# Performance work log

Measured on AMD Instinct MI355X. Metric: run time of the kernel, lower is better.

The kernel has to match this reference:

```python
import jax, jax.numpy as jnp
import numpy as np

NUM_EXPERTS = 16
TOP_K = 2
D_IN = 1024
D_HID = 4096
D_OUT = 1024
BATCH = 8192


def setup_inputs() -> dict:
    key = jax.random.key(0)
    ks = jax.random.split(key, 6)
    s_in = 1.0 / np.sqrt(D_IN)
    s_hid = 1.0 / np.sqrt(D_HID)
    return {
        "x": jax.random.normal(ks[0], (BATCH, D_IN), dtype=jnp.float32),
        "Wg": jax.random.normal(ks[1], (D_IN, NUM_EXPERTS), dtype=jnp.float32) * s_in,
        "W1": jax.random.normal(ks[2], (NUM_EXPERTS, D_IN, D_HID), dtype=jnp.float32) * s_in,
        "b1": jnp.zeros((NUM_EXPERTS, D_HID), dtype=jnp.float32),
        "W2": jax.random.normal(ks[3], (NUM_EXPERTS, D_HID, D_OUT), dtype=jnp.float32) * s_hid,
        "b2": jnp.zeros((NUM_EXPERTS, D_OUT), dtype=jnp.float32),
    }


def _moe_forward(x, Wg, W1, b1, W2, b2):
    # Gating: top-k routing with softmax over the selected logits.
    logits = x @ Wg                                   # [B, E]
    top_vals, top_idx = jax.lax.top_k(logits, TOP_K)  # [B, k]
    routing_weights = jax.nn.softmax(top_vals, axis=-1)  # [B, k]

    # Per-token combine weight for each expert (sum over k slots):
    # cw[b, e] = sum_k routing_weights[b, k] * (top_idx[b, k] == e)
    one_hot = jax.nn.one_hot(top_idx, NUM_EXPERTS, dtype=x.dtype)  # [B, k, E]
    combine_w = jnp.einsum("bk,bke->be", routing_weights, one_hot)  # [B, E]

    # Per-expert MLP compute + weighted scatter-add combine.
    # Fixed-size loop over experts (structurally distinct weight slices);
    # equivalent math to the original's gather/compute/scatter dispatch.
    out = jnp.zeros((x.shape[0], D_OUT), dtype=x.dtype)
    for e in range(NUM_EXPERTS):
        h = jax.nn.relu(x @ W1[e] + b1[e])            # [B, H]
        y = h @ W2[e] + b2[e]                         # [B, O]
        out = out + combine_w[:, e:e + 1] * y
    return out


def reference(x, Wg, W1, b1, W2, b2):
    return _moe_forward(x, Wg, W1, b1, W2, b2)
```

## Files before the change

kernel.cpp:

```cpp
#include <hip/hip_runtime.h>
#include <cstdio>

#define DIN   1024
#define DHID  4096
#define DOUT  1024
#define NEXP  16
#define NTOK  8192
#define NPAIR (NTOK * 2)
#define PADMAX 20480
#define MAXTILES 80

typedef _Float16 h8 __attribute__((ext_vector_type(8)));
typedef _Float16 h4 __attribute__((ext_vector_type(4)));
typedef float    f4 __attribute__((ext_vector_type(4)));

#define C_CNT  0
#define C_POFF 16
#define C_CUR  32
#define C_NT   48
#define C_TE   64
#define C_TP   256

__device__ __forceinline__ void async16(const void* g, void* l) {
  __builtin_amdgcn_global_load_lds((const __attribute__((address_space(1))) void*)g,
                                   (__attribute__((address_space(3))) void*)l, 16, 0, 0);
}

__global__ void k_init(float* __restrict__ out, const float* __restrict__ x,
                       _Float16* __restrict__ x16, int* __restrict__ ptok,
                       float* __restrict__ pw, int* __restrict__ ctrl) {
  int i = blockIdx.x * 256 + threadIdx.x;
  ((f4*)out)[i] = (f4){0.f, 0.f, 0.f, 0.f};
  float4 v = ((const float4*)x)[i];
  h4 hv = {(_Float16)v.x, (_Float16)v.y, (_Float16)v.z, (_Float16)v.w};
  ((h4*)x16)[i] = hv;
  if (i < PADMAX) { ptok[i] = 0; pw[i] = 0.f; }
  if (i < 1024) ctrl[i] = 0;
}

__global__ void k_gate(const float* __restrict__ x, const float* __restrict__ wg,
                       int* __restrict__ te, float* __restrict__ tw,
                       int* __restrict__ ctrl) {
  int t = blockIdx.x * 4 + (threadIdx.x >> 6);
  int l = threadIdx.x & 63;
  const float* xr = x + (long)t * DIN;
  float acc[NEXP];
#pragma unroll
  for (int e = 0; e < NEXP; ++e) acc[e] = 0.f;
  for (int k = l; k < DIN; k += 64) {
    float xv = xr[k];
    const float4* wr = (const float4*)(wg + (long)k * NEXP);
    float4 a = wr[0], b = wr[1], c = wr[2], d = wr[3];
    acc[0]  += xv * a.x; acc[1]  += xv * a.y; acc[2]  += xv * a.z; acc[3]  += xv * a.w;
    acc[4]  += xv * b.x; acc[5]  += xv * b.y; acc[6]  += xv * b.z; acc[7]  += xv * b.w;
    acc[8]  += xv * c.x; acc[9]  += xv * c.y; acc[10] += xv * c.z; acc[11] += xv * c.w;
    acc[12] += xv * d.x; acc[13] += xv * d.y; acc[14] += xv * d.z; acc[15] += xv * d.w;
  }
#pragma unroll
  for (int off = 32; off > 0; off >>= 1) {
#pragma unroll
    for (int e = 0; e < NEXP; ++e) acc[e] += __shfl_xor(acc[e], off, 64);
  }
  if (l == 0) {
    float v0 = -1e30f; int e0 = 0;
#pragma unroll
    for (int e = 0; e < NEXP; ++e) if (acc[e] > v0) { v0 = acc[e]; e0 = e; }
    float v1 = -1e30f; int e1 = 0;
#pragma unroll
    for (int e = 0; e < NEXP; ++e) if (e != e0 && acc[e] > v1) { v1 = acc[e]; e1 = e; }
    float d = expf(v1 - v0);
    float den = 1.f / (1.f + d);
    te[2 * t] = e0;     tw[2 * t] = den;
    te[2 * t + 1] = e1; tw[2 * t + 1] = d * den;
    atomicAdd(&ctrl[C_CNT + e0], 1);
    atomicAdd(&ctrl[C_CNT + e1], 1);
  }
}

__global__ void k_scan(int* __restrict__ ctrl) {
  if (threadIdx.x != 0) return;
  int off = 0, nt = 0;
  for (int e = 0; e < NEXP; ++e) {
    int c = ctrl[C_CNT + e];
    int tiles = (c + 255) >> 8;
    ctrl[C_POFF + e] = off;
    ctrl[C_CUR + e] = off;
    for (int i = 0; i < tiles; ++i) { ctrl[C_TE + nt] = e; ctrl[C_TP + nt] = off + i * 256; ++nt; }
    off += tiles * 256;
  }
  ctrl[C_NT] = nt;
}

__global__ void k_assign(const int* __restrict__ te, const float* __restrict__ tw,
                         int* __restrict__ ctrl, int* __restrict__ ptok,
                         float* __restrict__ pw) {
  int t = blockIdx.x * 256 + threadIdx.x;
#pragma unroll
  for (int s = 0; s < 2; ++s) {
    int e = te[2 * t + s];
    int pos = atomicAdd(&ctrl[C_CUR + e], 1);
    ptok[pos] = t;
    pw[pos] = tw[2 * t + s];
  }
}

__global__ void k_transpose(const float* __restrict__ W, _Float16* __restrict__ out,
                            int R, int C) {
  __shared__ __align__(16) _Float16 tile[64][136];
  int e = blockIdx.z;
  const float* Wb = W + ((long)e * R + blockIdx.x * 128) * C + blockIdx.y * 64;
  int tid = threadIdx.x;
  int rr = tid >> 4;
  int cc = (tid & 15) * 4;
#pragma unroll
  for (int i = 0; i < 8; ++i) {
    int r = rr + i * 16;
    float4 v = *(const float4*)(Wb + (long)r * C + cc);
    tile[cc + 0][r] = (_Float16)v.x;
    tile[cc + 1][r] = (_Float16)v.y;
    tile[cc + 2][r] = (_Float16)v.z;
    tile[cc + 3][r] = (_Float16)v.w;
  }
  __syncthreads();
  _Float16* ob = out + ((long)e * C + blockIdx.y * 64) * R + blockIdx.x * 128;
  int c2 = tid >> 4;
  int ch = tid & 15;
#pragma unroll
  for (int i = 0; i < 4; ++i) {
    int c = c2 + i * 16;
    *(h8*)(ob + (long)c * R + ch * 8) = *(const h8*)&tile[c][ch * 8];
  }
}

template<int KD, int ND, int G1>
__global__ __launch_bounds__(512, 2)
void k_gemm(const _Float16* __restrict__ A, const _Float16* __restrict__ Wt,
            const float* __restrict__ bias, const int* __restrict__ ctrl,
            const int* __restrict__ ptok, const float* __restrict__ pw,
            _Float16* __restrict__ Hout, float* __restrict__ out) {
  __shared__ __align__(16) _Float16 sm[65536];

  int mt = blockIdx.y;
  if (mt >= ctrl[C_NT]) return;
  int e  = ctrl[C_TE + mt];
  int p0 = ctrl[C_TP + mt];
  int n0 = blockIdx.x * 256;
  int tid = threadIdx.x;
  int w = tid >> 6, l = tid & 63;
  int wm = w & 1, wn = w >> 1;
  int ln15 = l & 15, lq = l >> 4;

  const _Float16* agp[4];
  const _Float16* bgp[4];
#pragma unroll
  for (int h = 0; h < 2; ++h)
#pragma unroll
    for (int j = 0; j < 2; ++j) {
      int r = (w * 2 + j) * 8 + (l >> 3);
      int c = (l & 7) ^ (r & 7);
      long arow = G1 ? (long)ptok[p0 + h * 128 + r] : (long)(p0 + h * 128 + r);
      agp[h * 2 + j] = A + arow * KD + c * 8;
      bgp[h * 2 + j] = Wt + ((long)e * ND + n0 + h * 128 + r) * KD + c * 8;
    }

  auto stageH = [&](int t, int half) {
    _Float16* dst = sm + (t & 1) * 32768 + (half & 1) * 16384 + (half >> 1) * 8192
                    + w * 1024;
    long koff = (long)t * 64;
    const _Float16* const* gp = (half & 1) ? bgp : agp;
#pragma unroll
    for (int j = 0; j < 2; ++j)
      async16(gp[(half >> 1) * 2 + j] + koff, dst + j * 512);
  };

  f4 acc[2][4][2][2];
#pragma unroll
  for (int mq = 0; mq < 2; ++mq)
#pragma unroll
    for (int i = 0; i < 4; ++i)
#pragma unroll
      for (int nq = 0; nq < 2; ++nq)
#pragma unroll
        for (int j = 0; j < 2; ++j) acc[mq][i][nq][j] = (f4){0.f, 0.f, 0.f, 0.f};

  h8 af[8], bf0[4], bf1[4];

  auto readA = [&](int d, int mq) {
    const _Float16* Ab = sm + d * 32768 + mq * 8192;
#pragma unroll
    for (int i = 0; i < 4; ++i) {
      int rh = wm * 64 + i * 16 + ln15;
#pragma unroll
      for (int ks = 0; ks < 2; ++ks)
        af[i * 2 + ks] = *(const h8*)&Ab[rh * 64 + (((ks * 4 + lq)) ^ (rh & 7)) * 8];
    }
  };
  auto readB = [&](int d, int nq, h8* bf) {
    const _Float16* Bb = sm + d * 32768 + 16384 + nq * 8192;
#pragma unroll
    for (int j = 0; j < 2; ++j) {
      int rh = wn * 32 + j * 16 + ln15;
#pragma unroll
      for (int ks = 0; ks < 2; ++ks)
        bf[j * 2 + ks] = *(const h8*)&Bb[rh * 64 + (((ks * 4 + lq)) ^ (rh & 7)) * 8];
    }
  };
  auto mfmaQ = [&](int mq, int nq, const h8* bf) {
    __builtin_amdgcn_s_setprio(1);
#pragma unroll
    for (int ks = 0; ks < 2; ++ks)
#pragma unroll
      for (int i = 0; i < 4; ++i)
#pragma unroll
        for (int j = 0; j < 2; ++j)
          acc[mq][i][nq][j] = __builtin_amdgcn_mfma_f32_16x16x32_f16(
              af[i * 2 + ks], bf[j * 2 + ks], acc[mq][i][nq][j], 0, 0, 0);
    __builtin_amdgcn_s_setprio(0);
  };

  constexpr int KSTEPS = KD / 64;

  stageH(0, 0); stageH(0, 1); stageH(0, 2); stageH(0, 3);
  stageH(1, 0); stageH(1, 1); stageH(1, 2);
  asm volatile("s_waitcnt vmcnt(6)" ::: "memory");
  __builtin_amdgcn_s_barrier();

#pragma unroll 2
  for (int t = 0; t < KSTEPS; ++t) {
    int d = t & 1;
    readA(d, 0);
    readB(d, 0, bf0);
    if (t + 1 < KSTEPS) stageH(t + 1, 3);
    __builtin_amdgcn_s_barrier();
    asm volatile("s_waitcnt lgkmcnt(0)" ::: "memory");
    mfmaQ(0, 0, bf0);
    __builtin_amdgcn_s_barrier();
    readB(d, 1, bf1);
    if (t + 2 < KSTEPS) stageH(t + 2, 0);
    __builtin_amdgcn_s_barrier();
    asm volatile("s_waitcnt lgkmcnt(0)" ::: "memory");
    mfmaQ(0, 1, bf1);
    __builtin_amdgcn_s_barrier();
    readA(d, 1);
    if (t + 2 < KSTEPS) stageH(t + 2, 1);
    __builtin_amdgcn_s_barrier();
    asm volatile("s_waitcnt lgkmcnt(0)" ::: "memory");
    mfmaQ(1, 1, bf1);
    __builtin_amdgcn_s_barrier();
    if (t + 2 < KSTEPS) stageH(t + 2, 2);
    if (t + 1 < KSTEPS) {
      if (t + 2 < KSTEPS) asm volatile("s_waitcnt vmcnt(6)" ::: "memory");
      else                asm volatile("s_waitcnt vmcnt(0)" ::: "memory");
    }
    __builtin_amdgcn_s_barrier();
    mfmaQ(1, 0, bf0);
    __builtin_amdgcn_s_barrier();
  }

  float bj[2][2];
#pragma unroll
  for (int nq = 0; nq < 2; ++nq)
#pragma unroll
    for (int j = 0; j < 2; ++j)
      bj[nq][j] = bias[e * ND + n0 + nq * 128 + wn * 32 + j * 16 + ln15];

  if (G1) {
    _Float16* cs = sm;
#pragma unroll
    for (int mq = 0; mq < 2; ++mq) {
      if (mq) __syncthreads();
#pragma unroll
      for (int i = 0; i < 4; ++i)
#pragma unroll
        for (int reg = 0; reg < 4; ++reg) {
          int row = wm * 64 + i * 16 + lq * 4 + reg;
#pragma unroll
          for (int nq = 0; nq < 2; ++nq)
#pragma unroll
            for (int j = 0; j < 2; ++j)
              cs[row * 264 + nq * 128 + wn * 32 + j * 16 + ln15] =
                  (_Float16)fmaxf(acc[mq][i][nq][j][reg] + bj[nq][j], 0.f);
        }
      __syncthreads();
#pragma unroll
      for (int p = 0; p < 8; ++p) {
        int idx = p * 512 + tid;
        int row = idx >> 5, ch = idx & 31;
        *(h8*)(Hout + (long)(p0 + mq * 128 + row) * DHID + n0 + ch * 8) =
            *(const h8*)&cs[row * 264 + ch * 8];
      }
    }
  } else {
#pragma unroll
    for (int mq = 0; mq < 2; ++mq)
#pragma unroll
      for (int i = 0; i < 4; ++i)
#pragma unroll
        for (int reg = 0; reg < 4; ++reg) {
          int p = p0 + mq * 128 + wm * 64 + i * 16 + lq * 4 + reg;
          float wgt = pw[p];
          if (wgt != 0.f) {
            int tk = ptok[p];
            float* orow = out + (long)tk * DOUT + n0;
#pragma unroll
            for (int nq = 0; nq < 2; ++nq)
#pragma unroll
              for (int j = 0; j < 2; ++j)
                atomicAdd(&orow[nq * 128 + wn * 32 + j * 16 + ln15],
                          wgt * (acc[mq][i][nq][j][reg] + bj[nq][j]));
          }
        }
  }
}

extern "C" void kernel_launch(void* const* d_in, const int* in_sizes, int n_in,
                              void* d_out, int out_size, void* d_ws, size_t ws_size,
                              hipStream_t stream) {
  const float* x  = (const float*)d_in[0];
  const float* Wg = (const float*)d_in[1];
  const float* W1 = (const float*)d_in[2];
  const float* b1 = (const float*)d_in[3];
  const float* W2 = (const float*)d_in[4];
  const float* b2 = (const float*)d_in[5];
  float* out = (float*)d_out;
  char* ws = (char*)d_ws;

  size_t WT_OFF = 0;
  size_t H_OFF  = WT_OFF + (size_t)NEXP * DHID * DIN * 2;
  size_t X_OFF  = H_OFF  + (size_t)PADMAX * DHID * 2;
  size_t TE_OFF = X_OFF  + (size_t)NTOK * DIN * 2;
  size_t TW_OFF = TE_OFF + (size_t)NPAIR * 4;
  size_t PT_OFF = TW_OFF + (size_t)NPAIR * 4;
  size_t PW_OFF = PT_OFF + (size_t)PADMAX * 4;
  size_t CT_OFF = PW_OFF + (size_t)PADMAX * 4;
  size_t END    = CT_OFF + 4096;
  if (ws_size < END) {
    fprintf(stderr, "kernel_launch: ws too small (%zu < %zu)\n", ws_size, END);
    return;
  }
  _Float16* Wt  = (_Float16*)(ws + WT_OFF);
  _Float16* H   = (_Float16*)(ws + H_OFF);
  _Float16* x16 = (_Float16*)(ws + X_OFF);
  int*   te   = (int*)(ws + TE_OFF);
  float* tw   = (float*)(ws + TW_OFF);
  int*   pt   = (int*)(ws + PT_OFF);
  float* pw   = (float*)(ws + PW_OFF);
  int*   ctrl = (int*)(ws + CT_OFF);

  k_init<<<NTOK * DIN / (256 * 4), 256, 0, stream>>>(out, x, x16, pt, pw, ctrl);
  k_gate<<<NTOK / 4, 256, 0, stream>>>(x, Wg, te, tw, ctrl);
  k_scan<<<1, 64, 0, stream>>>(ctrl);
  k_assign<<<NTOK / 256, 256, 0, stream>>>(te, tw, ctrl, pt, pw);

  k_transpose<<<dim3(DIN / 128, DHID / 64, NEXP), 256, 0, stream>>>(W1, Wt, DIN, DHID);
  k_gemm<DIN, DHID, 1><<<dim3(DHID / 256, MAXTILES), 512, 0, stream>>>(
      x16, Wt, b1, ctrl, pt, pw, H, nullptr);

  k_transpose<<<dim3(DHID / 128, DOUT / 64, NEXP), 256, 0, stream>>>(W2, Wt, DHID, DOUT);
  k_gemm<DHID, DOUT, 0><<<dim3(DOUT / 256, MAXTILES), 512, 0, stream>>>(
      H, Wt, b2, ctrl, pt, pw, nullptr, out);
}
```

Measured before the change: 1.289 ms.

## Split-K second expert GEMM, remap grid to 1D with XCD swizzle, parallelize scan

The second GEMM (K=4096, N=1024) is split four ways along K, which quadruples its block count so more CUs are busy. Partial sums go into the output through the existing weighted atomic scatter, and the bias is added only by the kp==0 slice. Both GEMMs now launch on a 1D grid whose block index is swizzled across eight groups, which changes how work lands on the XCDs and how well L2 is reused. The scan kernel now writes its tile table in parallel instead of from one thread. The split adds extra atomic traffic to the fp32 output and changes the order of the floating-point accumulation.

```diff
diff --git a/kernel.cpp b/kernel.cpp
--- a/kernel.cpp
+++ b/kernel.cpp
@@ -78,17 +78,30 @@
 }
 
 __global__ void k_scan(int* __restrict__ ctrl) {
-  if (threadIdx.x != 0) return;
-  int off = 0, nt = 0;
-  for (int e = 0; e < NEXP; ++e) {
-    int c = ctrl[C_CNT + e];
-    int tiles = (c + 255) >> 8;
-    ctrl[C_POFF + e] = off;
-    ctrl[C_CUR + e] = off;
-    for (int i = 0; i < tiles; ++i) { ctrl[C_TE + nt] = e; ctrl[C_TP + nt] = off + i * 256; ++nt; }
-    off += tiles * 256;
-  }
-  ctrl[C_NT] = nt;
+  __shared__ int sOff[NEXP], sT0[NEXP], sTiles[NEXP];
+  int tid = threadIdx.x;
+  if (tid == 0) {
+    int off = 0, nt = 0;
+    for (int e = 0; e < NEXP; ++e) {
+      int c = ctrl[C_CNT + e];
+      int tiles = (c + 255) >> 8;
+      ctrl[C_POFF + e] = off;
+      ctrl[C_CUR + e] = off;
+      sOff[e] = off; sT0[e] = nt; sTiles[e] = tiles;
+      nt += tiles;
+      off += tiles * 256;
+    }
+    ctrl[C_NT] = nt;
+  }
+  __syncthreads();
+  int nt = sT0[NEXP - 1] + sTiles[NEXP - 1];
+  for (int j = tid; j < nt; j += blockDim.x) {
+    int e = 0;
+#pragma unroll
+    for (int k = 1; k < NEXP; ++k) if (j >= sT0[k]) e = k;
+    ctrl[C_TE + j] = e;
+    ctrl[C_TP + j] = sOff[e] + (j - sT0[e]) * 256;
+  }
 }
 
 __global__ void k_assign(const int* __restrict__ te, const float* __restrict__ tw,
@@ -132,7 +145,7 @@
   }
 }
 
-template<int KD, int ND, int G1>
+template<int KD, int ND, int G1, int KP>
 __global__ __launch_bounds__(512, 2)
 void k_gemm(const _Float16* __restrict__ A, const _Float16* __restrict__ Wt,
             const float* __restrict__ bias, const int* __restrict__ ctrl,
@@ -140,11 +153,20 @@
             _Float16* __restrict__ Hout, float* __restrict__ out) {
   __shared__ __align__(16) _Float16 sm[65536];
 
-  int mt = blockIdx.y;
+  constexpr int NW = (ND / 256) * KP * MAXTILES;
+  constexpr int QX = NW / 8;
+  int bid = blockIdx.x;
+  int wid = (bid & 7) * QX + (bid >> 3);
+  int mt = wid % MAXTILES;
+  int g  = wid / MAXTILES;
+  int kp = (KP > 1) ? (g % KP) : 0;
+  int nb = g / KP;
+
   if (mt >= ctrl[C_NT]) return;
   int e  = ctrl[C_TE + mt];
   int p0 = ctrl[C_TP + mt];
-  int n0 = blockIdx.x * 256;
+  int n0 = nb * 256;
+  long kbase = (long)kp * (KD / KP);
   int tid = threadIdx.x;
   int w = tid >> 6, l = tid & 63;
   int wm = w & 1, wn = w >> 1;
@@ -159,8 +181,8 @@
       int r = (w * 2 + j) * 8 + (l >> 3);
       int c = (l & 7) ^ (r & 7);
       long arow = G1 ? (long)ptok[p0 + h * 128 + r] : (long)(p0 + h * 128 + r);
-      agp[h * 2 + j] = A + arow * KD + c * 8;
-      bgp[h * 2 + j] = Wt + ((long)e * ND + n0 + h * 128 + r) * KD + c * 8;
+      agp[h * 2 + j] = A + arow * KD + kbase + c * 8;
+      bgp[h * 2 + j] = Wt + ((long)e * ND + n0 + h * 128 + r) * KD + kbase + c * 8;
     }
 
   auto stageH = [&](int t, int half) {
@@ -218,7 +240,7 @@
     __builtin_amdgcn_s_setprio(0);
   };
 
-  constexpr int KSTEPS = KD / 64;
+  constexpr int KSTEPS = KD / 64 / KP;
 
   stageH(0, 0); stageH(0, 1); stageH(0, 2); stageH(0, 3);
   stageH(1, 0); stageH(1, 1); stageH(1, 2);
@@ -263,6 +285,12 @@
 #pragma unroll
     for (int j = 0; j < 2; ++j)
       bj[nq][j] = bias[e * ND + n0 + nq * 128 + wn * 32 + j * 16 + ln15];
+  if (KP > 1 && kp != 0) {
+#pragma unroll
+    for (int nq = 0; nq < 2; ++nq)
+#pragma unroll
+      for (int j = 0; j < 2; ++j) bj[nq][j] = 0.f;
+  }
 
   if (G1) {
     _Float16* cs = sm;
@@ -349,14 +377,14 @@
 
   k_init<<<NTOK * DIN / (256 * 4), 256, 0, stream>>>(out, x, x16, pt, pw, ctrl);
   k_gate<<<NTOK / 4, 256, 0, stream>>>(x, Wg, te, tw, ctrl);
-  k_scan<<<1, 64, 0, stream>>>(ctrl);
+  k_scan<<<1, 256, 0, stream>>>(ctrl);
   k_assign<<<NTOK / 256, 256, 0, stream>>>(te, tw, ctrl, pt, pw);
 
   k_transpose<<<dim3(DIN / 128, DHID / 64, NEXP), 256, 0, stream>>>(W1, Wt, DIN, DHID);
-  k_gemm<DIN, DHID, 1><<<dim3(DHID / 256, MAXTILES), 512, 0, stream>>>(
+  k_gemm<DIN, DHID, 1, 1><<<dim3((DHID / 256) * MAXTILES), 512, 0, stream>>>(
       x16, Wt, b1, ctrl, pt, pw, H, nullptr);
 
   k_transpose<<<dim3(DHID / 128, DOUT / 64, NEXP), 256, 0, stream>>>(W2, Wt, DHID, DOUT);
-  k_gemm<DHID, DOUT, 0><<<dim3(DOUT / 256, MAXTILES), 512, 0, stream>>>(
+  k_gemm<DHID, DOUT, 0, 4><<<dim3((DOUT / 256) * 4 * MAXTILES), 512, 0, stream>>>(
       H, Wt, b2, ctrl, pt, pw, nullptr, out);
 }
```

Result: slower. 1.357 ms (+5.3%).
